# Performance work log

Measured on AMD Instinct MI355X. Metric: run time of the kernel, lower is better.

The kernel has to match this reference:

```python
import jax, jax.numpy as jnp
import numpy as np

EPS = 1e-5
NEG = jnp.float32(-1e30)
SPP_LEVEL = 3
SPATIAL_SCALE = 0.125


def conv2d(x, w, b, pad):
    out = jax.lax.conv_general_dilated(x, w, (1, 1), [(pad, pad), (pad, pad)],
                                       dimension_numbers=('NCHW', 'OIHW', 'NCHW'))
    return out + b[None, :, None, None]


def bn2d(x, g, b):  # BatchNorm2d, training-mode batch stats (biased var), as in torch forward
    m = x.mean((0, 2, 3), keepdims=True)
    v = x.var((0, 2, 3), keepdims=True)
    return (x - m) * jax.lax.rsqrt(v + EPS) * g[None, :, None, None] + b[None, :, None, None]


def bn1d(x, g, b):
    m = x.mean(0)
    v = x.var(0)
    return (x - m) * jax.lax.rsqrt(v + EPS) * g + b


def maxpool2(x):
    return jax.lax.reduce_window(x, -jnp.inf, jax.lax.max, (1, 1, 2, 2), (1, 1, 2, 2), 'VALID')


def roi_spp(feat, roi):
    # feat: (B,C,Hf,Wf); roi: (R,5) int [im,x1,y1,x2,y2] in input-image coords.
    im = roi[:, 0].astype(jnp.int32)
    s = (roi[:, 1:].astype(jnp.float32) * SPATIAL_SCALE).astype(jnp.int32)  # trunc, coords >= 0
    c1, r1, c2, r2 = s[:, 0], s[:, 1], s[:, 2], s[:, 3]
    R = roi.shape[0]
    Hf, Wf = feat.shape[2], feat.shape[3]
    rows = jnp.arange(Hf)
    cols = jnp.arange(Wf)
    rmask = (rows[None, :] >= r1[:, None]) & (rows[None, :] <= r2[:, None])  # (R,Hf)
    w = c2 - c1 + 1
    froi = feat[im]  # (R,C,Hf,Wf)
    pieces = []
    for l in range(1, SPP_LEVEL + 1):  # adaptive_max_pool2d to (1,l) per level
        k = jnp.arange(l)
        lo = c1[:, None] + (k[None, :] * w[:, None]) // l
        hi = c1[:, None] + ((k[None, :] + 1) * w[:, None] + l - 1) // l - 1
        cmask = (cols[None, None, :] >= lo[:, :, None]) & (cols[None, None, :] <= hi[:, :, None])  # (R,l,Wf)
        mask = rmask[:, None, :, None] & cmask[:, :, None, :]  # (R,l,Hf,Wf)
        vals = jnp.where(mask[:, None], froi[:, :, None], NEG)  # (R,C,l,Hf,Wf)
        pieces.append(vals.max((-2, -1)).reshape(R, -1))  # channel-major flatten, like torch .view
    return jnp.concatenate(pieces, axis=1)  # (R, C*(1+2+3)) = (R, 3072)


def _forward(x, phocTensor, roi,
             c1w, c1b, g1, b1, c2w, c2b, g2, b2, c3w, c3b, g3, b3,
             c4w, c4b, g4, b4, c5w, c5b, g5, b5,
             f1w, f1b, g6, b6, f2w, f2b, g7, b7):
    out = jnp.pad(x, ((0, 0), (0, 0), (2, 2), (2, 2)), mode='edge')  # replicate pad
    out = maxpool2(jax.nn.relu(bn2d(conv2d(out, c1w, c1b, 0), g1, b1)))
    out = maxpool2(jax.nn.relu(bn2d(conv2d(out, c2w, c2b, 2), g2, b2)))
    out = jax.nn.relu(bn2d(conv2d(out, c3w, c3b, 1), g3, b3))
    out = maxpool2(jax.nn.relu(bn2d(conv2d(out, c4w, c4b, 1), g4, b4)))
    out = jax.nn.relu(bn2d(conv2d(out, c5w, c5b, 1), g5, b5))  # (B,512,6,16)
    out = roi_spp(out, roi)  # (R,3072)
    out = jax.nn.relu(bn1d(out @ f1w.T + f1b, g6, b6))
    out = jnp.concatenate([out, phocTensor], axis=1)  # (R, 2048+5853)
    out = jax.nn.relu(bn1d(out @ f2w.T + f2b, g7, b7))
    return out


def setup_inputs() -> dict:
    key = jax.random.key(0)
    ks = jax.random.split(key, 24)
    B, R = 64, 256
    x = jax.random.normal(ks[0], (B, 1, 48, 128), jnp.float32)
    # ROIs [im, x1, y1, x2, y2], guaranteed non-empty after /8 scaling
    im = jax.random.randint(ks[1], (R,), 0, B)
    x1 = jax.random.randint(ks[2], (R,), 0, 64)
    x2 = jnp.minimum(x1 + jax.random.randint(ks[3], (R,), 32, 64), 127)
    y1 = jax.random.randint(ks[4], (R,), 0, 16)
    y2 = jnp.minimum(y1 + jax.random.randint(ks[5], (R,), 16, 32), 47)
    roi = jnp.stack([im, x1, y1, x2, y2], axis=1).astype(jnp.int32)
    phocTensor = jax.random.uniform(ks[6], (R, 5853), jnp.float32)

    def he(k, shape):
        fan_in = int(np.prod(shape[1:]))
        return jax.random.normal(k, shape, jnp.float32) * np.sqrt(2.0 / fan_in).astype(np.float32)

    d = {'x': x, 'roi': roi, 'phocTensor': phocTensor}
    conv_shapes = [('c1', (64, 1, 5, 5)), ('c2', (128, 64, 5, 5)), ('c3', (256, 128, 3, 3)),
                   ('c4', (512, 256, 3, 3)), ('c5', (512, 512, 3, 3))]
    for i, (nm, sh) in enumerate(conv_shapes):
        d[nm + 'w'] = he(ks[7 + i], sh)
        d[nm + 'b'] = jnp.zeros((sh[0],), jnp.float32)
        d['g' + str(i + 1)] = jnp.ones((sh[0],), jnp.float32)
        d['b' + str(i + 1)] = jnp.zeros((sh[0],), jnp.float32)
    d['f1w'] = he(ks[12], (2048, 3072)); d['f1b'] = jnp.zeros((2048,), jnp.float32)
    d['g6'] = jnp.ones((2048,), jnp.float32); d['b6'] = jnp.zeros((2048,), jnp.float32)
    d['f2w'] = he(ks[13], (2048, 2048 + 5853)); d['f2b'] = jnp.zeros((2048,), jnp.float32)
    d['g7'] = jnp.ones((2048,), jnp.float32); d['b7'] = jnp.zeros((2048,), jnp.float32)
    return d


def reference(x, roi, phocTensor,
              c1w, c1b, g1, b1, c2w, c2b, g2, b2, c3w, c3b, g3, b3,
              c4w, c4b, g4, b4, c5w, c5b, g5, b5,
              f1w, f1b, g6, b6, f2w, f2b, g7, b7):
    return _forward(x, phocTensor, roi,
                    c1w, c1b, g1, b1, c2w, c2b, g2, b2, c3w, c3b, g3, b3,
                    c4w, c4b, g4, b4, c5w, c5b, g5, b5,
                    f1w, f1b, g6, b6, f2w, f2b, g7, b7)
```

## Files before the change

kernel.cpp:

```cpp
#include <hip/hip_runtime.h>
#include <hip/hip_bf16.h>


typedef __bf16 bf16;
using bf16x4 = __attribute__((ext_vector_type(4))) __bf16;
using bf16x8 = __attribute__((ext_vector_type(8))) __bf16;
using f32x4  = __attribute__((ext_vector_type(4))) float;

__device__ __forceinline__ void split2(float v, bf16& h, bf16& l) {
  bf16 hb = (bf16)v;
  h = hb;
  l = (bf16)(v - (float)hb);
}

__device__ __forceinline__ int iclamp(int v, int lo, int hi) {
  return v < lo ? lo : (v > hi ? hi : v);
}

__device__ __forceinline__ size_t pk_off(int row, int k, int Kd64) {
  return ((size_t)(row >> 4) * Kd64 + (k >> 6)) * 1024 +
         (size_t)(((k >> 5) & 1) * 512 + ((k >> 3) & 3) * 128 + ((row & 15) << 3) + (k & 7));
}

__device__ __forceinline__ void gld_lds16(const bf16* g, void* lds) {
  __builtin_amdgcn_global_load_lds(
      (const __attribute__((address_space(1))) unsigned int*)g,
      (__attribute__((address_space(3))) unsigned int*)lds, 16, 0, 0);
}

__device__ __forceinline__ void wconv_tx(const float* __restrict__ w,
                                         bf16* __restrict__ oh_,
                                         bf16* __restrict__ ol_,
                                         int CI, int KS, int i, int total) {
  if (i >= total) return;
  int ci = i % CI; int t = i / CI; int kw = t % KS; t /= KS; int kh = t % KS; int co = t / KS;
  float v = w[(((size_t)co * CI + ci) * KS + kh) * KS + kw];
  bf16 h, l; split2(v, h, l);
  oh_[i] = h;
  if (ol_) ol_[i] = l;
}

__global__ __launch_bounds__(256) void prep_k(const float* __restrict__ c2w,
                                              const float* __restrict__ c3w,
                                              const float* __restrict__ c4w,
                                              const float* __restrict__ c5w,
                                              const float* __restrict__ f1w,
                                              const float* __restrict__ f2w,
                                              const float* __restrict__ phoc,
                                              bf16* __restrict__ Wc2h,
                                              bf16* __restrict__ Wc3h,
                                              bf16* __restrict__ Wc4h,
                                              bf16* __restrict__ Wc5h,
                                              bf16* __restrict__ Wc5l,
                                              bf16* __restrict__ Wf1,
                                              bf16* __restrict__ Wf2,
                                              bf16* __restrict__ cch,
                                              bf16* __restrict__ ccl) {
  int b = blockIdx.x;
  int tid = threadIdx.x;
  if (b < 800)  { wconv_tx(c2w, Wc2h, nullptr, 64, 5, b * 256 + tid, 204800); return; }
  b -= 800;
  if (b < 1152) { wconv_tx(c3w, Wc3h, nullptr, 128, 3, b * 256 + tid, 294912); return; }
  b -= 1152;
  if (b < 4608) { wconv_tx(c4w, Wc4h, nullptr, 256, 3, b * 256 + tid, 1179648); return; }
  b -= 4608;
  if (b < 9216) { wconv_tx(c5w, Wc5h, Wc5l, 512, 3, b * 256 + tid, 2359296); return; }
  b -= 9216;
  if (b < 6144) {
    int i = b * 256 + tid;
    int k0 = (i % 768) * 4, n = i / 768;
    const float4 v = *(const float4*)(f1w + (size_t)n * 3072 + k0);
    bf16x4 o = { (bf16)v.x, (bf16)v.y, (bf16)v.z, (bf16)v.w };
    *(bf16x4*)(Wf1 + pk_off(n, k0, 48)) = o;
    return;
  }
  b -= 6144;
  if (b < 16384) {
    int i = b * 256 + tid;
    int k0 = (i & 2047) * 4, n = i >> 11;
    const float* xp = f2w + (size_t)n * 7901 + k0;
    bf16x4 o;
#pragma unroll
    for (int j = 0; j < 4; j++) o[j] = (bf16)((k0 + j < 7901) ? xp[j] : 0.f);
    *(bf16x4*)(Wf2 + pk_off(n, k0, 128)) = o;
    return;
  }
  b -= 16384;
  {
    int i = b * 256 + tid;
    if (i >= 256 * 6144) return;
    int k = i % 6144, r = i / 6144;
    int col = 2048 + k;
    float v = (col < 7901) ? phoc[(size_t)r * 5853 + (col - 2048)] : 0.f;
    bf16 h, l; split2(v, h, l);
    size_t o = pk_off(r, col, 128);
    cch[o] = h;
    ccl[o] = l;
  }
}

__global__ __launch_bounds__(256) void conv1_stats_k(const float* __restrict__ x,
                                                     const float* __restrict__ wt,
                                                     float* __restrict__ part) {
  int co0 = blockIdx.y * 8;
  float sums[8] = {0.f}, sqs[8] = {0.f};
  for (int r = 0; r < 16; r++) {
    int pix = blockIdx.x * 4096 + r * 256 + threadIdx.x;
    int w = pix & 127; int t = pix >> 7; int h = t % 48; int n = t / 48;
    const float* ip = x + (size_t)n * 48 * 128;
    int ihs[5], iws[5];
#pragma unroll
    for (int k = 0; k < 5; k++) {
      ihs[k] = iclamp(h + k - 2, 0, 47);
      iws[k] = iclamp(w + k - 2, 0, 127);
    }
    float win[25];
#pragma unroll
    for (int kh = 0; kh < 5; kh++)
#pragma unroll
      for (int kw = 0; kw < 5; kw++) win[kh * 5 + kw] = ip[ihs[kh] * 128 + iws[kw]];
#pragma unroll
    for (int j = 0; j < 8; j++) {
      const float* wp = wt + (size_t)(co0 + j) * 25;
      float acc = 0.f;
#pragma unroll
      for (int k = 0; k < 25; k++) acc += win[k] * wp[k];
      sums[j] += acc; sqs[j] += acc * acc;
    }
  }
  __shared__ float ls[256], lq[256];
  for (int j = 0; j < 8; j++) {
    ls[threadIdx.x] = sums[j]; lq[threadIdx.x] = sqs[j];
    __syncthreads();
    for (int o = 128; o > 0; o >>= 1) {
      if (threadIdx.x < o) { ls[threadIdx.x] += ls[threadIdx.x + o]; lq[threadIdx.x] += lq[threadIdx.x + o]; }
      __syncthreads();
    }
    if (threadIdx.x == 0) {
      int c = co0 + j;
      part[((size_t)c * 96 + blockIdx.x) * 2 + 0] = ls[0];
      part[((size_t)c * 96 + blockIdx.x) * 2 + 1] = lq[0];
    }
    __syncthreads();
  }
}

__global__ __launch_bounds__(256) void conv1_apply_k(const float* __restrict__ x,
                                                     const float* __restrict__ wt,
                                                     const float* __restrict__ scale,
                                                     const float* __restrict__ shift,
                                                     bf16* __restrict__ yh,
                                                     bf16* __restrict__ yl) {
  int i = blockIdx.x * 256 + threadIdx.x;
  if (i >= 64 * 28 * 68) return;
  int owp = i % 68; int t = i / 68; int ohp = t % 28; int n = t / 28;
  int co0 = blockIdx.y * 8;
  int oh = ohp - 2, ow = owp - 2;
  bf16x8 hv, lv;
#pragma unroll
  for (int j = 0; j < 8; j++) { hv[j] = (bf16)0.f; lv[j] = (bf16)0.f; }
  if (oh >= 0 && oh < 24 && ow >= 0 && ow < 64) {
    const float* ip = x + (size_t)n * 48 * 128;
    int shr[6], swc[6];
#pragma unroll
    for (int k = 0; k < 6; k++) {
      shr[k] = iclamp(2 * oh + k - 2, 0, 47);
      swc[k] = iclamp(2 * ow + k - 2, 0, 127);
    }
    float win[36];
#pragma unroll
    for (int r = 0; r < 6; r++)
#pragma unroll
      for (int c = 0; c < 6; c++) win[r * 6 + c] = ip[shr[r] * 128 + swc[c]];
#pragma unroll
    for (int j = 0; j < 8; j++) {
      const float* wp = wt + (size_t)(co0 + j) * 25;
      float sc = scale[co0 + j], sh = shift[co0 + j];
      float m = -1e30f;
#pragma unroll
      for (int dy = 0; dy < 2; dy++)
#pragma unroll
        for (int dx = 0; dx < 2; dx++) {
          float acc = 0.f;
#pragma unroll
          for (int kh = 0; kh < 5; kh++)
#pragma unroll
            for (int kw = 0; kw < 5; kw++)
              acc += win[(kh + dy) * 6 + kw + dx] * wp[kh * 5 + kw];
          m = fmaxf(m, acc * sc + sh);
        }
      float v = fmaxf(m, 0.f);
      bf16 h, l; split2(v, h, l);
      hv[j] = h; lv[j] = l;
    }
  }
  size_t o = (size_t)i * 64 + co0;
  *(bf16x8*)(yh + o) = hv;
  *(bf16x8*)(yl + o) = lv;
}

__global__ __launch_bounds__(256) void conv2_gemm_k(const bf16* __restrict__ Ahi,
                                                    const bf16* __restrict__ Bhi,
                                                    float* __restrict__ Wmax,
                                                    float* __restrict__ Wmin,
                                                    float* __restrict__ part) {
  __shared__ bf16 Ash[416 * 64];
  __shared__ bf16 Bsh[128 * 64];
  __shared__ float red[2][128][8];
  const int t = threadIdx.x;
  const int lane = t & 63, w = t >> 6;
  const int m0 = blockIdx.x * 128;
  const int img = m0 / 1536;
  const int oh0 = (m0 % 1536) >> 6;
  const size_t abase = ((size_t)(img * 28 + oh0) * 68) * 64;

#pragma unroll
  for (int i = 0; i < 13; i++) {
    int f = i * 256 + t;
    int p = f >> 3; if (p > 407) p = 407;
    int s = f & 7;
    int ss = s ^ (p & 7);
    gld_lds16(Ahi + abase + (size_t)p * 64 + ss * 8,
              (char*)Ash + (size_t)(i * 256 + w * 64) * 16);
  }

  size_t boff[4];
#pragma unroll
  for (int i = 0; i < 4; i++) {
    int f = (i * 4 + w) * 64 + lane;
    int row = f >> 3, slot = f & 7;
    int ss = slot ^ (row & 7);
    boff[i] = (size_t)row * 1600 + ss * 8;
  }

  const int wrow = w >> 1, wcol = w & 1;
  const int kg = lane >> 4, l15 = lane & 15;
  int pixb[4];
#pragma unroll
  for (int q = 0; q < 4; q++) pixb[q] = wrow * 68 + q * 16 + l15;
  int brb[4], bmk[4];
#pragma unroll
  for (int q = 0; q < 4; q++) {
    int rb = wcol * 64 + q * 16 + l15;
    brb[q] = rb * 128; bmk[q] = rb & 7;
  }
  const char* Ashb = (const char*)Ash;
  const char* Bshb = (const char*)Bsh;

  f32x4 acc[4][4] = {};
  for (int kc = 0; kc < 25; ++kc) {
    const int kh = kc / 5, kw = kc % 5;
    const int kofs = kh * 68 + kw;
    const int k0 = kc * 64;
#pragma unroll
    for (int i = 0; i < 4; i++)
      gld_lds16(Bhi + boff[i] + k0, (char*)Bsh + (i * 4 + w) * 1024);
    __syncthreads();
#pragma unroll
    for (int ks = 0; ks < 2; ks++) {
      const int slot = ks * 4 + kg;
      bf16x8 ah[4], bh[4];
#pragma unroll
      for (int q = 0; q < 4; q++) {
        int pix = pixb[q] + kofs;
        ah[q] = *(const bf16x8*)(Ashb + pix * 128 + ((slot ^ (pix & 7)) << 4));
        bh[q] = *(const bf16x8*)(Bshb + brb[q] + ((slot ^ bmk[q]) << 4));
      }
#pragma unroll
      for (int mi = 0; mi < 4; mi++)
#pragma unroll
        for (int ni = 0; ni < 4; ni++)
          acc[mi][ni] = __builtin_amdgcn_mfma_f32_16x16x32_bf16(ah[mi], bh[ni], acc[mi][ni], 0, 0, 0);
    }
    __syncthreads();
  }

  const int ccol = l15;
  float hmx[4][4][2], hmn[4][4][2];
#pragma unroll
  for (int mi = 0; mi < 4; mi++)
#pragma unroll
    for (int ni = 0; ni < 4; ni++)
#pragma unroll
      for (int jp = 0; jp < 2; jp++) {
        float a = acc[mi][ni][2 * jp], b = acc[mi][ni][2 * jp + 1];
        hmx[mi][ni][jp] = fmaxf(a, b);
        hmn[mi][ni][jp] = fminf(a, b);
      }
  const int contrib = kg * 2 + wrow;
#pragma unroll
  for (int ni = 0; ni < 4; ni++) {
    float s = 0.f, q = 0.f;
#pragma unroll
    for (int mi = 0; mi < 4; mi++)
#pragma unroll
      for (int jj = 0; jj < 4; jj++) {
        float v = acc[mi][ni][jj];
        s += v; q += v * v;
      }
    int coll = wcol * 64 + ni * 16 + ccol;
    red[0][coll][contrib] = s;
    red[1][coll][contrib] = q;
  }
  float* exch = (float*)Ash;
  if (wrow == 1) {
    float* ep = exch + (size_t)(wcol * 64 + lane) * 64;
#pragma unroll
    for (int mi = 0; mi < 4; mi++)
#pragma unroll
      for (int ni = 0; ni < 4; ni++)
#pragma unroll
        for (int jp = 0; jp < 2; jp++) {
          int s = (mi * 8 + ni * 2 + jp) * 2;
          ep[s + 0] = hmx[mi][ni][jp];
          ep[s + 1] = hmn[mi][ni][jp];
        }
  }
  __syncthreads();
  if (wrow == 0) {
    const float* ep = exch + (size_t)(wcol * 64 + lane) * 64;
    const int pmb = img * 384 + (oh0 >> 1) * 32;
#pragma unroll
    for (int mi = 0; mi < 4; mi++)
#pragma unroll
      for (int ni = 0; ni < 4; ni++)
#pragma unroll
        for (int jp = 0; jp < 2; jp++) {
          int s = (mi * 8 + ni * 2 + jp) * 2;
          float mx = fmaxf(hmx[mi][ni][jp], ep[s + 0]);
          float mn = fminf(hmn[mi][ni][jp], ep[s + 1]);
          int pm = pmb + mi * 8 + kg * 2 + jp;
          int ch = wcol * 64 + ni * 16 + ccol;
          Wmax[(size_t)pm * 128 + ch] = mx;
          Wmin[(size_t)pm * 128 + ch] = mn;
        }
  }
  if (t < 128) {
    float s = 0.f, q = 0.f;
#pragma unroll
    for (int j = 0; j < 8; j++) { s += red[0][t][j]; q += red[1][t][j]; }
    size_t c = t;
    part[(c * gridDim.x + blockIdx.x) * 2 + 0] = s;
    part[(c * gridDim.x + blockIdx.x) * 2 + 1] = q;
  }
}

template<int CI, int KS, int OH, int OW, int CO, bool ALO, bool BLO, int SPLIT, bool FUSEPOOL>
__global__ __launch_bounds__(256) void conv_gemm_k(const bf16* __restrict__ Ahi,
                                                   const bf16* __restrict__ Alo,
                                                   const bf16* __restrict__ Bhi,
                                                   const bf16* __restrict__ Blo,
                                                   float* __restrict__ Cout,
                                                   float* __restrict__ Cmin,
                                                   float* __restrict__ part) {
  static_assert(CI % 64 == 0, "chunk must not straddle ci segments");
  static_assert(!FUSEPOOL || (OW == 32 && SPLIT == 1), "fusepool needs OW=32");
  constexpr int K = KS * KS * CI;
  constexpr int IWP = OW + KS - 1;
  constexpr int NCH = K / 64;
  static_assert(NCH % SPLIT == 0, "split must divide chunk count");
  constexpr int NCHS = NCH / SPLIT;
  constexpr int M = 64 * OH * OW;
  __shared__ bf16 Ash[128 * 64];
  __shared__ bf16 Asl[ALO ? 128 * 64 : 64];
  __shared__ bf16 Bsh[128 * 64];
  __shared__ bf16 Bsl[BLO ? 128 * 64 : 64];
  __shared__ float red[2][128][8];
  const int t = threadIdx.x;
  const int lane = t & 63, w = t >> 6;
  const int m0 = blockIdx.x * 128, n0 = blockIdx.y * 128;
  const int z = (SPLIT > 1) ? blockIdx.z : 0;

  int apix[4]; size_t boff[4];
#pragma unroll
  for (int i = 0; i < 4; i++) {
    int f = (i * 4 + w) * 64 + lane;
    int row = f >> 3, slot = f & 7;
    int ss = slot ^ (row & 7);
    int m = m0 + row;
    int n = m / (OH * OW); int rem = m % (OH * OW);
    int oh = rem / OW, ow_ = rem % OW;
    apix[i] = ((n * (OH + KS - 1) + oh) * IWP + ow_) * CI + ss * 8;
    boff[i] = (size_t)(n0 + row) * K + ss * 8;
  }

  const int wrow = w >> 1, wcol = w & 1;
  const int kg = lane >> 4, l15 = lane & 15;
  int arb[4], amk[4], brb[4], bmk[4];
#pragma unroll
  for (int q = 0; q < 4; q++) {
    int ra = wrow * 64 + q * 16 + l15;
    arb[q] = ra * 128; amk[q] = ra & 7;
    int rb = wcol * 64 + q * 16 + l15;
    brb[q] = rb * 128; bmk[q] = rb & 7;
  }
  const char* Ashb = (const char*)Ash;
  const char* Aslb = (const char*)Asl;
  const char* Bshb = (const char*)Bsh;
  const char* Bslb = (const char*)Bsl;

  f32x4 acc[4][4] = {};
  for (int kc = z * NCHS; kc < (z + 1) * NCHS; ++kc) {
    const int k0 = kc * 64;
    const int seg = k0 / CI;
    const int ci0 = k0 % CI;
    const int kh = seg / KS, kw = seg % KS;
    const int aoff = (kh * IWP + kw) * CI + ci0;
#pragma unroll
    for (int i = 0; i < 4; i++) {
      gld_lds16(Ahi + (size_t)apix[i] + aoff, (char*)Ash + (i * 4 + w) * 1024);
      if (ALO)
        gld_lds16(Alo + (size_t)apix[i] + aoff, (char*)Asl + (i * 4 + w) * 1024);
      gld_lds16(Bhi + boff[i] + k0,   (char*)Bsh + (i * 4 + w) * 1024);
      if (BLO)
        gld_lds16(Blo + boff[i] + k0, (char*)Bsl + (i * 4 + w) * 1024);
    }
    __syncthreads();
#pragma unroll
    for (int ks = 0; ks < 2; ks++) {
      const int slot = ks * 4 + kg;
      bf16x8 ah[4], bh[4];
#pragma unroll
      for (int q = 0; q < 4; q++) {
        ah[q] = *(const bf16x8*)(Ashb + arb[q] + ((slot ^ amk[q]) << 4));
        bh[q] = *(const bf16x8*)(Bshb + brb[q] + ((slot ^ bmk[q]) << 4));
      }
#pragma unroll
      for (int mi = 0; mi < 4; mi++)
#pragma unroll
        for (int ni = 0; ni < 4; ni++)
          acc[mi][ni] = __builtin_amdgcn_mfma_f32_16x16x32_bf16(ah[mi], bh[ni], acc[mi][ni], 0, 0, 0);
      if (ALO) {
        bf16x8 al[4];
#pragma unroll
        for (int q = 0; q < 4; q++)
          al[q] = *(const bf16x8*)(Aslb + arb[q] + ((slot ^ amk[q]) << 4));
#pragma unroll
        for (int mi = 0; mi < 4; mi++)
#pragma unroll
          for (int ni = 0; ni < 4; ni++)
            acc[mi][ni] = __builtin_amdgcn_mfma_f32_16x16x32_bf16(al[mi], bh[ni], acc[mi][ni], 0, 0, 0);
      }
      if (BLO) {
        bf16x8 bl[4];
#pragma unroll
        for (int q = 0; q < 4; q++)
          bl[q] = *(const bf16x8*)(Bslb + brb[q] + ((slot ^ bmk[q]) << 4));
#pragma unroll
        for (int mi = 0; mi < 4; mi++)
#pragma unroll
          for (int ni = 0; ni < 4; ni++)
            acc[mi][ni] = __builtin_amdgcn_mfma_f32_16x16x32_bf16(ah[mi], bl[ni], acc[mi][ni], 0, 0, 0);
      }
    }
    __syncthreads();
  }

  const int crow0 = kg * 4, ccol = l15;
  if constexpr (FUSEPOOL) {
    const int n_img = m0 / (OH * OW);
    const int oh0 = (m0 % (OH * OW)) / OW;
    const int pmb = n_img * (OH / 2) * (OW / 2) + (oh0 / 2 + wrow) * (OW / 2);
#pragma unroll
    for (int mi = 0; mi < 2; mi++)
#pragma unroll
      for (int ni = 0; ni < 4; ni++)
#pragma unroll
        for (int jp = 0; jp < 2; jp++) {
          float a0 = acc[mi][ni][2 * jp],     a1 = acc[mi][ni][2 * jp + 1];
          float b0 = acc[mi + 2][ni][2 * jp], b1 = acc[mi + 2][ni][2 * jp + 1];
          float mx = fmaxf(fmaxf(a0, a1), fmaxf(b0, b1));
          float mn = fminf(fminf(a0, a1), fminf(b0, b1));
          int pm = pmb + mi * 8 + kg * 2 + jp;
          int ch = n0 + wcol * 64 + ni * 16 + ccol;
          Cout[(size_t)pm * CO + ch] = mx;
          Cmin[(size_t)pm * CO + ch] = mn;
        }
  } else {
    float* Cz = Cout + (size_t)z * M * CO;
#pragma unroll
    for (int mi = 0; mi < 4; mi++) {
      int m = m0 + wrow * 64 + mi * 16 + crow0;
#pragma unroll
      for (int ni = 0; ni < 4; ni++) {
        int nn = n0 + wcol * 64 + ni * 16 + ccol;
        float* cp = Cz + (size_t)m * CO + nn;
#pragma unroll
        for (int jj = 0; jj < 4; jj++) cp[(size_t)jj * CO] = acc[mi][ni][jj];
      }
    }
  }
  if constexpr (SPLIT == 1) {
    const int contrib = kg * 2 + wrow;
#pragma unroll
    for (int ni = 0; ni < 4; ni++) {
      float s = 0.f, q = 0.f;
#pragma unroll
      for (int mi = 0; mi < 4; mi++)
#pragma unroll
        for (int jj = 0; jj < 4; jj++) {
          float v = acc[mi][ni][jj];
          s += v; q += v * v;
        }
      int coll = wcol * 64 + ni * 16 + ccol;
      red[0][coll][contrib] = s;
      red[1][coll][contrib] = q;
    }
    __syncthreads();
    if (t < 128) {
      float s = 0.f, q = 0.f;
#pragma unroll
      for (int j = 0; j < 8; j++) { s += red[0][t][j]; q += red[1][t][j]; }
      size_t c = n0 + t;
      part[(c * gridDim.x + blockIdx.x) * 2 + 0] = s;
      part[(c * gridDim.x + blockIdx.x) * 2 + 1] = q;
    }
  }
}

template<int K, int SPLIT>
__global__ __launch_bounds__(256) void fc_gemm_k(const bf16* __restrict__ Ahp,
                                                 const bf16* __restrict__ Alp,
                                                 const bf16* __restrict__ Bhp,
                                                 float* __restrict__ Cout) {
  constexpr int Kd64 = K / 64;
  constexpr int NCHS = Kd64 / SPLIT;
  constexpr int M = 256, N = 2048;
  const int t = threadIdx.x;
  const int lane = t & 63, w = t >> 6;
  const int m0 = blockIdx.x * 128, n0 = blockIdx.y * 128;
  const int z = blockIdx.z;
  const int wrow = w >> 1, wcol = w & 1;
  const int kg = lane >> 4, l15 = lane & 15;

  size_t ab[4], bb[4];
#pragma unroll
  for (int q = 0; q < 4; q++) {
    int rbA = (m0 >> 4) + wrow * 4 + q;
    ab[q] = (size_t)rbA * Kd64 * 1024 + (size_t)lane * 8;
    int rbB = (n0 >> 4) + wcol * 4 + q;
    bb[q] = (size_t)rbB * Kd64 * 1024 + (size_t)lane * 8;
  }

  f32x4 acc[4][4] = {};
  for (int kc = z * NCHS; kc < (z + 1) * NCHS; ++kc) {
    const size_t bco = (size_t)kc * 1024;
#pragma unroll
    for (int ks = 0; ks < 2; ks++) {
      const size_t soff = bco + ks * 512;
      bf16x8 ah[4], al[4], bh[4];
#pragma unroll
      for (int q = 0; q < 4; q++) {
        ah[q] = *(const bf16x8*)(Ahp + ab[q] + soff);
        al[q] = *(const bf16x8*)(Alp + ab[q] + soff);
        bh[q] = *(const bf16x8*)(Bhp + bb[q] + soff);
      }
#pragma unroll
      for (int mi = 0; mi < 4; mi++)
#pragma unroll
        for (int ni = 0; ni < 4; ni++)
          acc[mi][ni] = __builtin_amdgcn_mfma_f32_16x16x32_bf16(ah[mi], bh[ni], acc[mi][ni], 0, 0, 0);
#pragma unroll
      for (int mi = 0; mi < 4; mi++)
#pragma unroll
        for (int ni = 0; ni < 4; ni++)
          acc[mi][ni] = __builtin_amdgcn_mfma_f32_16x16x32_bf16(al[mi], bh[ni], acc[mi][ni], 0, 0, 0);
    }
  }

  const int crow0 = kg * 4, ccol = l15;
  float* Cz = Cout + (size_t)z * M * N;
#pragma unroll
  for (int mi = 0; mi < 4; mi++) {
    int m = m0 + wrow * 64 + mi * 16 + crow0;
#pragma unroll
    for (int ni = 0; ni < 4; ni++) {
      int nn = n0 + wcol * 64 + ni * 16 + ccol;
      float* cp = Cz + (size_t)m * N + nn;
#pragma unroll
      for (int jj = 0; jj < 4; jj++) cp[(size_t)jj * N] = acc[mi][ni][jj];
    }
  }
}

template<int M, int CO, int SPLIT, int NS>
__global__ __launch_bounds__(256) void reduce_bn_k(const float* __restrict__ Cp,
                                                   float* __restrict__ Cf,
                                                   float* __restrict__ part) {
  int c = blockIdx.x * 64 + (threadIdx.x & 63);
  int rl = threadIdx.x >> 6;
  constexpr int ROWS = M / NS;
  int r0 = blockIdx.y * ROWS;
  float sum = 0.f, sq = 0.f;
  for (int r = r0 + rl; r < r0 + ROWS; r += 4) {
    float v = 0.f;
#pragma unroll
    for (int s = 0; s < SPLIT; s++) v += Cp[(size_t)s * M * CO + (size_t)r * CO + c];
    Cf[(size_t)r * CO + c] = v;
    sum += v; sq += v * v;
  }
  __shared__ float ls[256], lq[256];
  ls[threadIdx.x] = sum; lq[threadIdx.x] = sq;
  __syncthreads();
  if (threadIdx.x < 64) {
    sum = ls[threadIdx.x] + ls[threadIdx.x + 64] + ls[threadIdx.x + 128] + ls[threadIdx.x + 192];
    sq  = lq[threadIdx.x] + lq[threadIdx.x + 64] + lq[threadIdx.x + 128] + lq[threadIdx.x + 192];
    part[((size_t)c * NS + blockIdx.y) * 2 + 0] = sum;
    part[((size_t)c * NS + blockIdx.y) * 2 + 1] = sq;
  }
}

__global__ __launch_bounds__(64) void bn_finalize(const float* __restrict__ part,
                                                  const float* __restrict__ g,
                                                  const float* __restrict__ b,
                                                  float* __restrict__ scale,
                                                  float* __restrict__ shift,
                                                  int S, float invCount) {
  int c = blockIdx.x;
  int lane = threadIdx.x;
  float sum = 0.f, sq = 0.f;
  for (int s = lane; s < S; s += 64) {
    sum += part[((size_t)c * S + s) * 2 + 0];
    sq  += part[((size_t)c * S + s) * 2 + 1];
  }
#pragma unroll
  for (int o = 32; o > 0; o >>= 1) {
    sum += __shfl_xor(sum, o);
    sq  += __shfl_xor(sq, o);
  }
  if (lane == 0) {
    float m = sum * invCount;
    float var = sq * invCount - m * m;
    float sc = g[c] * rsqrtf(var + 1e-5f);
    scale[c] = sc;
    shift[c] = b[c] - m * sc;
  }
}

template<int CO, int IH, int IW, int PADO>
__global__ __launch_bounds__(256) void bn_act_pad_k(const float* __restrict__ x,
                                                    const float* __restrict__ scale,
                                                    const float* __restrict__ shift,
                                                    bf16* __restrict__ yh,
                                                    bf16* __restrict__ yl) {
  constexpr int OHP = IH + 2 * PADO, OWP = IW + 2 * PADO;
  constexpr int CO8 = CO / 8;
  int i = blockIdx.x * 256 + threadIdx.x;
  if (i >= 64 * OHP * OWP * CO8) return;
  int c8 = i % CO8; int t = i / CO8; int owp = t % OWP; t /= OWP; int ohp = t % OHP; int n = t / OHP;
  int c0 = c8 * 8;
  int oh = ohp - PADO, ow = owp - PADO;
  bf16x8 hv, lv;
#pragma unroll
  for (int j = 0; j < 8; j++) { hv[j] = (bf16)0.f; lv[j] = (bf16)0.f; }
  if (oh >= 0 && oh < IH && ow >= 0 && ow < IW) {
    float sc[8], sh[8];
    *(f32x4*)(sc)     = *(const f32x4*)(scale + c0);
    *(f32x4*)(sc + 4) = *(const f32x4*)(scale + c0 + 4);
    *(f32x4*)(sh)     = *(const f32x4*)(shift + c0);
    *(f32x4*)(sh + 4) = *(const f32x4*)(shift + c0 + 4);
    const float* p = x + (((size_t)(n * IH) + oh) * IW + ow) * CO + c0;
    float ta[8];
    *(f32x4*)(ta) = *(const f32x4*)(p); *(f32x4*)(ta + 4) = *(const f32x4*)(p + 4);
#pragma unroll
    for (int j = 0; j < 8; j++) {
      float vv = fmaxf(ta[j] * sc[j] + sh[j], 0.f);
      bf16 h, l; split2(vv, h, l);
      hv[j] = h; lv[j] = l;
    }
  }
  size_t o = (size_t)i * 8;
  *(bf16x8*)(yh + o) = hv;
  *(bf16x8*)(yl + o) = lv;
}

template<int CO, int PH, int PW, int PADO>
__global__ __launch_bounds__(256) void act_pool_pad_k(const float* __restrict__ wmax,
                                                      const float* __restrict__ wmin,
                                                      const float* __restrict__ scale,
                                                      const float* __restrict__ shift,
                                                      bf16* __restrict__ yh,
                                                      bf16* __restrict__ yl) {
  constexpr int OHP = PH + 2 * PADO, OWP = PW + 2 * PADO;
  constexpr int CO8 = CO / 8;
  int i = blockIdx.x * 256 + threadIdx.x;
  if (i >= 64 * OHP * OWP * CO8) return;
  int c8 = i % CO8; int t = i / CO8; int owp = t % OWP; t /= OWP; int ohp = t % OHP; int n = t / OHP;
  int c0 = c8 * 8;
  int oh = ohp - PADO, ow = owp - PADO;
  bf16x8 hv, lv;
#pragma unroll
  for (int j = 0; j < 8; j++) { hv[j] = (bf16)0.f; lv[j] = (bf16)0.f; }
  if (oh >= 0 && oh < PH && ow >= 0 && ow < PW) {
    float sc[8], sh[8], mx[8], mn[8];
    *(f32x4*)(sc)     = *(const f32x4*)(scale + c0);
    *(f32x4*)(sc + 4) = *(const f32x4*)(scale + c0 + 4);
    *(f32x4*)(sh)     = *(const f32x4*)(shift + c0);
    *(f32x4*)(sh + 4) = *(const f32x4*)(shift + c0 + 4);
    size_t off = (((size_t)(n * PH) + oh) * PW + ow) * CO + c0;
    *(f32x4*)(mx)     = *(const f32x4*)(wmax + off);
    *(f32x4*)(mx + 4) = *(const f32x4*)(wmax + off + 4);
    *(f32x4*)(mn)     = *(const f32x4*)(wmin + off);
    *(f32x4*)(mn + 4) = *(const f32x4*)(wmin + off + 4);
#pragma unroll
    for (int j = 0; j < 8; j++) {
      float sel = (sc[j] >= 0.f) ? mx[j] : mn[j];
      float vv = fmaxf(sel * sc[j] + sh[j], 0.f);
      bf16 h, l; split2(vv, h, l);
      hv[j] = h; lv[j] = l;
    }
  }
  size_t o = (size_t)i * 8;
  *(bf16x8*)(yh + o) = hv;
  *(bf16x8*)(yl + o) = lv;
}

__global__ __launch_bounds__(256) void spp_k(const float* __restrict__ feat,
                                             const float* __restrict__ scale,
                                             const float* __restrict__ shift,
                                             const int* __restrict__ roi,
                                             bf16* __restrict__ oh_,
                                             bf16* __restrict__ ol_) {
  int c = blockIdx.x * 256 + threadIdx.x;
  int r = blockIdx.y;
  const int* rp = roi + r * 5;
  int im = rp[0];
  int c1 = rp[1] >> 3, r1 = rp[2] >> 3, c2 = rp[3] >> 3, r2 = rp[4] >> 3;
  int w = c2 - c1 + 1;
  int lo[6], hi[6];
  int bi = 0;
#pragma unroll
  for (int l = 1; l <= 3; l++)
    for (int k = 0; k < l; k++) {
      lo[bi] = c1 + (k * w) / l;
      hi[bi] = c1 + ((k + 1) * w + l - 1) / l - 1;
      bi++;
    }
  float mx[6];
#pragma unroll
  for (int b = 0; b < 6; b++) mx[b] = -1e30f;
  float sc = scale[c], sh = shift[c];
  const float* fp = feat + (size_t)im * 96 * 512 + c;
  for (int row = r1; row <= r2; row++)
    for (int col = c1; col <= c2; col++) {
      float v = fp[(size_t)(row * 16 + col) * 512] * sc + sh;
#pragma unroll
      for (int b = 0; b < 6; b++)
        if (col >= lo[b] && col <= hi[b]) mx[b] = fmaxf(mx[b], v);
    }
  int idx[6] = {c, 512 + c * 2, 512 + c * 2 + 1, 1536 + c * 3, 1536 + c * 3 + 1, 1536 + c * 3 + 2};
#pragma unroll
  for (int b = 0; b < 6; b++) {
    float v = fmaxf(mx[b], 0.f);
    bf16 h, l; split2(v, h, l);
    size_t o = pk_off(r, idx[b], 48);
    oh_[o] = h;
    ol_[o] = l;
  }
}

__global__ __launch_bounds__(256) void bn1d_apply_cc_k(const float* __restrict__ x,
                                                       const float* __restrict__ scale,
                                                       const float* __restrict__ shift,
                                                       bf16* __restrict__ ch,
                                                       bf16* __restrict__ cl) {
  int i = blockIdx.x * 256 + threadIdx.x;
  if (i >= 256 * 256) return;
  int f8 = i & 255, r = i >> 8;
  int f0 = f8 * 8;
  float xv[8], sc[8], sh[8];
  *(f32x4*)(xv)     = *(const f32x4*)(x + (size_t)r * 2048 + f0);
  *(f32x4*)(xv + 4) = *(const f32x4*)(x + (size_t)r * 2048 + f0 + 4);
  *(f32x4*)(sc)     = *(const f32x4*)(scale + f0);
  *(f32x4*)(sc + 4) = *(const f32x4*)(scale + f0 + 4);
  *(f32x4*)(sh)     = *(const f32x4*)(shift + f0);
  *(f32x4*)(sh + 4) = *(const f32x4*)(shift + f0 + 4);
  bf16x8 hv, lv;
#pragma unroll
  for (int j = 0; j < 8; j++) {
    float v = fmaxf(xv[j] * sc[j] + sh[j], 0.f);
    bf16 h, l; split2(v, h, l);
    hv[j] = h; lv[j] = l;
  }
  size_t o = pk_off(r, f0, 128);
  *(bf16x8*)(ch + o) = hv;
  *(bf16x8*)(cl + o) = lv;
}

__global__ __launch_bounds__(256) void bn1d_apply_f32_k(const float* __restrict__ x,
                                                        const float* __restrict__ scale,
                                                        const float* __restrict__ shift,
                                                        float* __restrict__ y) {
  int i = blockIdx.x * 256 + threadIdx.x;
  if (i >= 256 * 512) return;
  int f4 = i & 511, r = i >> 9;
  int f0 = f4 * 4;
  f32x4 xv = *(const f32x4*)(x + (size_t)r * 2048 + f0);
  f32x4 sc = *(const f32x4*)(scale + f0);
  f32x4 sh = *(const f32x4*)(shift + f0);
  f32x4 o;
#pragma unroll
  for (int j = 0; j < 4; j++) o[j] = fmaxf(xv[j] * sc[j] + sh[j], 0.f);
  *(f32x4*)(y + (size_t)r * 2048 + f0) = o;
}

extern "C" void kernel_launch(void* const* d_in, const int* in_sizes, int n_in,
                              void* d_out, int out_size, void* d_ws, size_t ws_size,
                              hipStream_t stream) {
  (void)in_sizes; (void)n_in; (void)out_size; (void)ws_size;

  const float* x    = (const float*)d_in[0];
  const int*   roi  = (const int*)  d_in[1];
  const float* phoc = (const float*)d_in[2];
  const float* c1w  = (const float*)d_in[3];
  const float* g1   = (const float*)d_in[5];
  const float* b1   = (const float*)d_in[6];
  const float* c2w  = (const float*)d_in[7];
  const float* g2   = (const float*)d_in[9];
  const float* b2   = (const float*)d_in[10];
  const float* c3w  = (const float*)d_in[11];
  const float* g3   = (const float*)d_in[13];
  const float* b3   = (const float*)d_in[14];
  const float* c4w  = (const float*)d_in[15];
  const float* g4   = (const float*)d_in[17];
  const float* b4   = (const float*)d_in[18];
  const float* c5w  = (const float*)d_in[19];
  const float* g5   = (const float*)d_in[21];
  const float* b5   = (const float*)d_in[22];
  const float* f1w  = (const float*)d_in[23];
  const float* g6   = (const float*)d_in[25];
  const float* b6   = (const float*)d_in[26];
  const float* f2w  = (const float*)d_in[27];
  const float* g7   = (const float*)d_in[29];
  const float* b7   = (const float*)d_in[30];
  float* out = (float*)d_out;

  char* ws = (char*)d_ws;
  bf16*  Ahi  = (bf16*) (ws + 0x0200000);
  bf16*  Alo  = (bf16*) (ws + 0x1200000);
  float* C    = (float*)(ws + 0x2200000);
  float* CMIN = (float*)(ws + 0x2E00000);
  float* C5F  = (float*)(ws + 0x4600000);
  bf16*  Wc2h = (bf16*) (ws + 0x5500000);
  bf16*  Wc3h = (bf16*) (ws + 0x5570000);
  bf16*  Wc4h = (bf16*) (ws + 0x5600000);
  bf16*  Wc5h = (bf16*) (ws + 0x5840000);
  bf16*  Wf1  = (bf16*) (ws + 0x5CC0000);
  bf16*  Wf2  = (bf16*) (ws + 0x68C0000);
  bf16*  Wc5l = (bf16*) (ws + 0x8C00000);
  bf16*  Shi  = (bf16*) (ws + 0x9080000);
  bf16*  Slo  = (bf16*) (ws + 0x9200000);
  float* G6   = (float*)(ws + 0x9380000);
  bf16*  CChi = (bf16*) (ws + 0x9580000);
  bf16*  CClo = (bf16*) (ws + 0x9980000);
  float* G7   = (float*)(ws + 0x9D80000);
  float* PART = (float*)(ws + 0x9F80000);
  float* SC   = (float*)(ws + 0xA040000);
  float* SH   = (float*)(ws + 0xA050000);

  prep_k<<<44448, 256, 0, stream>>>(c2w, c3w, c4w, c5w, f1w, f2w, phoc,
                                    Wc2h, Wc3h, Wc4h, Wc5h, Wc5l, Wf1, Wf2,
                                    CChi, CClo);

  conv1_stats_k<<<dim3(96, 8), 256, 0, stream>>>(x, c1w, PART);
  bn_finalize<<<64, 64, 0, stream>>>(PART, g1, b1, SC, SH, 96, 1.f / 393216.f);
  conv1_apply_k<<<dim3(476, 8), 256, 0, stream>>>(x, c1w, SC, SH, Ahi, Alo);

  conv2_gemm_k<<<768, 256, 0, stream>>>(Ahi, Wc2h, C, CMIN, PART);
  bn_finalize<<<128, 64, 0, stream>>>(PART, g2, b2, SC, SH, 768, 1.f / 98304.f);
  act_pool_pad_k<128, 12, 32, 1><<<1904, 256, 0, stream>>>(C, CMIN, SC, SH, Ahi, Alo);

  conv_gemm_k<128, 3, 12, 32, 256, true, false, 1, false><<<dim3(192, 2), 256, 0, stream>>>(Ahi, Alo, Wc3h, nullptr, C, nullptr, PART);
  bn_finalize<<<256, 64, 0, stream>>>(PART, g3, b3, SC, SH, 192, 1.f / 24576.f);
  bn_act_pad_k<256, 12, 32, 1><<<3808, 256, 0, stream>>>(C, SC, SH, Ahi, Alo);

  conv_gemm_k<256, 3, 12, 32, 512, false, false, 1, true><<<dim3(192, 4), 256, 0, stream>>>(Ahi, Alo, Wc4h, nullptr, C, CMIN, PART);
  bn_finalize<<<512, 64, 0, stream>>>(PART, g4, b4, SC, SH, 192, 1.f / 24576.f);
  act_pool_pad_k<512, 6, 16, 1><<<2304, 256, 0, stream>>>(C, CMIN, SC, SH, Ahi, Alo);

  conv_gemm_k<512, 3, 6, 16, 512, true, true, 2, false><<<dim3(48, 4, 2), 256, 0, stream>>>(Ahi, Alo, Wc5h, Wc5l, C, nullptr, nullptr);
  reduce_bn_k<6144, 512, 2, 16><<<dim3(8, 16), 256, 0, stream>>>(C, C5F, PART);
  bn_finalize<<<512, 64, 0, stream>>>(PART, g5, b5, SC, SH, 16, 1.f / 6144.f);

  spp_k<<<dim3(2, 256), 256, 0, stream>>>(C5F, SC, SH, roi, Shi, Slo);

  fc_gemm_k<3072, 16><<<dim3(2, 16, 16), 256, 0, stream>>>(Shi, Slo, Wf1, C);
  reduce_bn_k<256, 2048, 16, 4><<<dim3(32, 4), 256, 0, stream>>>(C, G6, PART);
  bn_finalize<<<2048, 64, 0, stream>>>(PART, g6, b6, SC, SH, 4, 1.f / 256.f);
  bn1d_apply_cc_k<<<256, 256, 0, stream>>>(G6, SC, SH, CChi, CClo);

  fc_gemm_k<8192, 16><<<dim3(2, 16, 16), 256, 0, stream>>>(CChi, CClo, Wf2, C);
  reduce_bn_k<256, 2048, 16, 4><<<dim3(32, 4), 256, 0, stream>>>(C, G7, PART);
  bn_finalize<<<2048, 64, 0, stream>>>(PART, g7, b7, SC, SH, 4, 1.f / 256.f);
  bn1d_apply_f32_k<<<512, 256, 0, stream>>>(G7, SC, SH, out);
}
```

Measured before the change: 577.3 us.

## Stage conv weight transposes through LDS and widen conv1 channel blocking

The conv weight re-layout in prep_k now uses one block per output channel. Each block reads that channel's weights contiguously into shared memory and writes them back transposed, replacing scattered per-element global gathers and shrinking the grid. conv1 stats and apply kernels each handle 16 output channels per thread instead of 8, halving the number of input window reloads. The stats reduction switches from a shared-memory tree with many barriers to wave shuffles. The cost is more registers in the conv1 kernels and fewer blocks.

```diff
diff --git a/kernel.cpp b/kernel.cpp
--- a/kernel.cpp
+++ b/kernel.cpp
@@ -26,18 +26,6 @@
   __builtin_amdgcn_global_load_lds(
       (const __attribute__((address_space(1))) unsigned int*)g,
       (__attribute__((address_space(3))) unsigned int*)lds, 16, 0, 0);
-}
-
-__device__ __forceinline__ void wconv_tx(const float* __restrict__ w,
-                                         bf16* __restrict__ oh_,
-                                         bf16* __restrict__ ol_,
-                                         int CI, int KS, int i, int total) {
-  if (i >= total) return;
-  int ci = i % CI; int t = i / CI; int kw = t % KS; t /= KS; int kh = t % KS; int co = t / KS;
-  float v = w[(((size_t)co * CI + ci) * KS + kh) * KS + kw];
-  bf16 h, l; split2(v, h, l);
-  oh_[i] = h;
-  if (ol_) ol_[i] = l;
 }
 
 __global__ __launch_bounds__(256) void prep_k(const float* __restrict__ c2w,
@@ -56,16 +44,33 @@
                                               bf16* __restrict__ Wf2,
                                               bf16* __restrict__ cch,
                                               bf16* __restrict__ ccl) {
+  __shared__ float buf[4608];
   int b = blockIdx.x;
   int tid = threadIdx.x;
-  if (b < 800)  { wconv_tx(c2w, Wc2h, nullptr, 64, 5, b * 256 + tid, 204800); return; }
-  b -= 800;
-  if (b < 1152) { wconv_tx(c3w, Wc3h, nullptr, 128, 3, b * 256 + tid, 294912); return; }
-  b -= 1152;
-  if (b < 4608) { wconv_tx(c4w, Wc4h, nullptr, 256, 3, b * 256 + tid, 1179648); return; }
-  b -= 4608;
-  if (b < 9216) { wconv_tx(c5w, Wc5h, Wc5l, 512, 3, b * 256 + tid, 2359296); return; }
-  b -= 9216;
+  const float* src = nullptr;
+  bf16 *dsth = nullptr, *dstl = nullptr;
+  int CI = 0, KK = 0, co = 0;
+  if (b < 128)        { src = c2w; dsth = Wc2h; CI = 64;  KK = 25; co = b; }
+  else if (b < 384)   { src = c3w; dsth = Wc3h; CI = 128; KK = 9;  co = b - 128; }
+  else if (b < 896)   { src = c4w; dsth = Wc4h; CI = 256; KK = 9;  co = b - 384; }
+  else if (b < 1408)  { src = c5w; dsth = Wc5h; dstl = Wc5l; CI = 512; KK = 9; co = b - 896; }
+  if (src) {
+    const int n = CI * KK;
+    const float* sp = src + (size_t)co * n;
+    for (int i = tid; i < n; i += 256) buf[i] = sp[i];
+    __syncthreads();
+    bf16* oh = dsth + (size_t)co * n;
+    bf16* ol = dstl ? dstl + (size_t)co * n : nullptr;
+    for (int o = tid; o < n; o += 256) {
+      int ci = o & (CI - 1), kk = o / CI;
+      float v = buf[ci * KK + kk];
+      bf16 h, l; split2(v, h, l);
+      oh[o] = h;
+      if (ol) ol[o] = l;
+    }
+    return;
+  }
+  b -= 1408;
   if (b < 6144) {
     int i = b * 256 + tid;
     int k0 = (i % 768) * 4, n = i / 768;
@@ -102,8 +107,8 @@
 __global__ __launch_bounds__(256) void conv1_stats_k(const float* __restrict__ x,
                                                      const float* __restrict__ wt,
                                                      float* __restrict__ part) {
-  int co0 = blockIdx.y * 8;
-  float sums[8] = {0.f}, sqs[8] = {0.f};
+  int co0 = blockIdx.y * 16;
+  float sums[16] = {0.f}, sqs[16] = {0.f};
   for (int r = 0; r < 16; r++) {
     int pix = blockIdx.x * 4096 + r * 256 + threadIdx.x;
     int w = pix & 127; int t = pix >> 7; int h = t % 48; int n = t / 48;
@@ -120,7 +125,7 @@
 #pragma unroll
       for (int kw = 0; kw < 5; kw++) win[kh * 5 + kw] = ip[ihs[kh] * 128 + iws[kw]];
 #pragma unroll
-    for (int j = 0; j < 8; j++) {
+    for (int j = 0; j < 16; j++) {
       const float* wp = wt + (size_t)(co0 + j) * 25;
       float acc = 0.f;
 #pragma unroll
@@ -128,20 +133,23 @@
       sums[j] += acc; sqs[j] += acc * acc;
     }
   }
-  __shared__ float ls[256], lq[256];
-  for (int j = 0; j < 8; j++) {
-    ls[threadIdx.x] = sums[j]; lq[threadIdx.x] = sqs[j];
-    __syncthreads();
-    for (int o = 128; o > 0; o >>= 1) {
-      if (threadIdx.x < o) { ls[threadIdx.x] += ls[threadIdx.x + o]; lq[threadIdx.x] += lq[threadIdx.x + o]; }
-      __syncthreads();
-    }
-    if (threadIdx.x == 0) {
-      int c = co0 + j;
-      part[((size_t)c * 96 + blockIdx.x) * 2 + 0] = ls[0];
-      part[((size_t)c * 96 + blockIdx.x) * 2 + 1] = lq[0];
-    }
-    __syncthreads();
+  __shared__ float wsum[4][16][2];
+  const int lane = threadIdx.x & 63, w4 = threadIdx.x >> 6;
+#pragma unroll
+  for (int j = 0; j < 16; j++) {
+    float s = sums[j], q = sqs[j];
+#pragma unroll
+    for (int o = 32; o > 0; o >>= 1) { s += __shfl_xor(s, o); q += __shfl_xor(q, o); }
+    if (lane == 0) { wsum[w4][j][0] = s; wsum[w4][j][1] = q; }
+  }
+  __syncthreads();
+  if (threadIdx.x < 16) {
+    int j = threadIdx.x;
+    float s = wsum[0][j][0] + wsum[1][j][0] + wsum[2][j][0] + wsum[3][j][0];
+    float q = wsum[0][j][1] + wsum[1][j][1] + wsum[2][j][1] + wsum[3][j][1];
+    int c = co0 + j;
+    part[((size_t)c * 96 + blockIdx.x) * 2 + 0] = s;
+    part[((size_t)c * 96 + blockIdx.x) * 2 + 1] = q;
   }
 }
 
@@ -154,11 +162,14 @@
   int i = blockIdx.x * 256 + threadIdx.x;
   if (i >= 64 * 28 * 68) return;
   int owp = i % 68; int t = i / 68; int ohp = t % 28; int n = t / 28;
-  int co0 = blockIdx.y * 8;
+  int co0 = blockIdx.y * 16;
   int oh = ohp - 2, ow = owp - 2;
-  bf16x8 hv, lv;
-#pragma unroll
-  for (int j = 0; j < 8; j++) { hv[j] = (bf16)0.f; lv[j] = (bf16)0.f; }
+  bf16x8 hv0, lv0, hv1, lv1;
+#pragma unroll
+  for (int j = 0; j < 8; j++) {
+    hv0[j] = (bf16)0.f; lv0[j] = (bf16)0.f;
+    hv1[j] = (bf16)0.f; lv1[j] = (bf16)0.f;
+  }
   if (oh >= 0 && oh < 24 && ow >= 0 && ow < 64) {
     const float* ip = x + (size_t)n * 48 * 128;
     int shr[6], swc[6];
@@ -173,7 +184,7 @@
 #pragma unroll
       for (int c = 0; c < 6; c++) win[r * 6 + c] = ip[shr[r] * 128 + swc[c]];
 #pragma unroll
-    for (int j = 0; j < 8; j++) {
+    for (int j = 0; j < 16; j++) {
       const float* wp = wt + (size_t)(co0 + j) * 25;
       float sc = scale[co0 + j], sh = shift[co0 + j];
       float m = -1e30f;
@@ -191,12 +202,15 @@
         }
       float v = fmaxf(m, 0.f);
       bf16 h, l; split2(v, h, l);
-      hv[j] = h; lv[j] = l;
+      if (j < 8) { hv0[j] = h; lv0[j] = l; }
+      else       { hv1[j - 8] = h; lv1[j - 8] = l; }
     }
   }
   size_t o = (size_t)i * 64 + co0;
-  *(bf16x8*)(yh + o) = hv;
-  *(bf16x8*)(yl + o) = lv;
+  *(bf16x8*)(yh + o)     = hv0;
+  *(bf16x8*)(yl + o)     = lv0;
+  *(bf16x8*)(yh + o + 8) = hv1;
+  *(bf16x8*)(yl + o + 8) = lv1;
 }
 
 __global__ __launch_bounds__(256) void conv2_gemm_k(const bf16* __restrict__ Ahi,
@@ -858,13 +872,13 @@
   float* SC   = (float*)(ws + 0xA040000);
   float* SH   = (float*)(ws + 0xA050000);
 
-  prep_k<<<44448, 256, 0, stream>>>(c2w, c3w, c4w, c5w, f1w, f2w, phoc,
+  prep_k<<<30080, 256, 0, stream>>>(c2w, c3w, c4w, c5w, f1w, f2w, phoc,
                                     Wc2h, Wc3h, Wc4h, Wc5h, Wc5l, Wf1, Wf2,
                                     CChi, CClo);
 
-  conv1_stats_k<<<dim3(96, 8), 256, 0, stream>>>(x, c1w, PART);
+  conv1_stats_k<<<dim3(96, 4), 256, 0, stream>>>(x, c1w, PART);
   bn_finalize<<<64, 64, 0, stream>>>(PART, g1, b1, SC, SH, 96, 1.f / 393216.f);
-  conv1_apply_k<<<dim3(476, 8), 256, 0, stream>>>(x, c1w, SC, SH, Ahi, Alo);
+  conv1_apply_k<<<dim3(476, 4), 256, 0, stream>>>(x, c1w, SC, SH, Ahi, Alo);
 
   conv2_gemm_k<<<768, 256, 0, stream>>>(Ahi, Wc2h, C, CMIN, PART);
   bn_finalize<<<128, 64, 0, stream>>>(PART, g2, b2, SC, SH, 768, 1.f / 98304.f);
```

Result: slower. 690.7 us (+19.6%).
